# Kernel tuning notes

Hardware: AMD Instinct MI355X
Metric: run time of the kernel (lower is better)

The kernel has to match this reference:

```python
import jax, jax.numpy as jnp
import numpy as np

N_BATCH, D_FEAT, N_CLASSES = 96, 64, 21
MARGIN = 0.3


def setup_inputs() -> dict:
    key = jax.random.key(0)
    k1, k2, k3 = jax.random.split(key, 3)
    logits = jax.random.normal(k1, (N_BATCH, D_FEAT), dtype=jnp.float32)
    feat2 = jax.random.normal(k2, (N_BATCH, D_FEAT), dtype=jnp.float32)
    labels = (jax.random.uniform(k3, (N_BATCH, N_CLASSES)) < 0.3).astype(jnp.float32)
    return {"logits": logits, "labels": labels, "feat2": feat2}


def reference(logits, labels, feat2):
    """Dense-mask formulation of QuadrupletMarginMiner (defaults:
    margin=0.3, type_of_quadruplets='all', what_is_hard='one').

    Instead of a data-dependent list of quadruplets, returns a boolean
    tensor valid[i, j, k, n] that is True exactly for the quadruplets the
    torch module would return (same set, dense encoding).
    """
    n = labels.shape[0]
    eps = 1e-12

    # --- label structure ------------------------------------------------
    s = (labels @ labels.T) > 0                      # share-a-label matrix
    diffs = ~s                                       # torch: sames ^ 1 (pre diag fill)
    sames = s & ~jnp.eye(n, dtype=bool)              # fill_diagonal_(0)
    jk_triu = jnp.triu(jnp.ones((n, n), dtype=bool), k=1)  # strict j < k

    # valid (I, J, K) triples: AP1 & AP2 & j<k   -> [n, n, n]
    triple = sames[:, :, None] & sames[:, None, :] & jk_triu[None, :, :]
    # attach every negative N: diffs[i, n]        -> [n, n, n, n]
    quad = triple[:, :, :, None] & diffs[:, None, None, :]

    # --- distances (negative cosine similarity) ---------------------------
    xn = logits / jnp.maximum(jnp.linalg.norm(logits, axis=1, keepdims=True), eps)
    yn = feat2 / jnp.maximum(jnp.linalg.norm(feat2, axis=1, keepdims=True), eps)
    mat = -(xn @ yn.T)                               # [n, n]

    # margin_p[i, p, neg] = mat[i, neg] - mat[i, p]  (p stands for J or K)
    margin_pn = mat[:, None, :] - mat[:, :, None]    # [i, p, neg]
    viol = margin_pn <= MARGIN                       # [i, p, neg] bool

    # 'all' quadruplets + 'one' hardness: (margin1 <= m) | (margin2 <= m)
    cond = viol[:, :, None, :] | viol[:, None, :, :]  # [i, j, k, neg]

    return quad & cond
```

## Files before the change

### kernel.cpp

```cpp
#include <hip/hip_runtime.h>
#include <math.h>

#define NB 96
#define NB2 (NB * NB)
#define DFEAT 64
#define NCLS 21
#define MARGIN 0.3

typedef int i4 __attribute__((ext_vector_type(4)));
typedef unsigned int u32;

__global__ void precompute_kernel(const float* __restrict__ logits,
                                  const float* __restrict__ labels,
                                  const float* __restrict__ feat2,
                                  double* __restrict__ mat,
                                  double* __restrict__ thr,
                                  unsigned char* __restrict__ share) {
    int gid = blockIdx.x * blockDim.x + threadIdx.x;
    if (gid >= NB2) return;
    int i = gid / NB;
    int j = gid - i * NB;

    const float* xi = logits + i * DFEAT;
    const float* yj = feat2 + j * DFEAT;
    double nx = 0.0, ny = 0.0, dot = 0.0;
#pragma unroll
    for (int d = 0; d < DFEAT; ++d) {
        double a = (double)xi[d];
        double b = (double)yj[d];
        nx += a * a;
        ny += b * b;
        dot += a * b;
    }
    nx = fmax(sqrt(nx), 1e-12);
    ny = fmax(sqrt(ny), 1e-12);
    double m = -(dot / (nx * ny));
    mat[gid] = m;
    thr[gid] = MARGIN + m;

    const float* li = labels + i * NCLS;
    const float* lj = labels + j * NCLS;
    float ldot = 0.f;
#pragma unroll
    for (int c = 0; c < NCLS; ++c) ldot += li[c] * lj[c];
    share[gid] = (ldot > 0.f) ? 1 : 0;
}

__global__ void mask_kernel(const double* __restrict__ mat,
                            const double* __restrict__ thr,
                            const unsigned char* __restrict__ share,
                            u32* __restrict__ mask4) {
    int gid = blockIdx.x * blockDim.x + threadIdx.x;
    if (gid >= NB2) return;
    int i = gid / NB;
    double t = thr[gid];
    const double* mrow = mat + i * NB;
    const unsigned char* srow = share + i * NB;
    u32 w0 = 0, w1 = 0, w2 = 0;
#pragma unroll
    for (int n = 0; n < 32; ++n)
        if (!srow[n] && (mrow[n] <= t)) w0 |= (1u << n);
#pragma unroll
    for (int n = 0; n < 32; ++n)
        if (!srow[32 + n] && (mrow[32 + n] <= t)) w1 |= (1u << n);
#pragma unroll
    for (int n = 0; n < 32; ++n)
        if (!srow[64 + n] && (mrow[64 + n] <= t)) w2 |= (1u << n);
    mask4[gid * 4 + 0] = w0;
    mask4[gid * 4 + 1] = w1;
    mask4[gid * 4 + 2] = w2;
    mask4[gid * 4 + 3] = 0;
}

__global__ __launch_bounds__(256) void quad_kernel(const double* __restrict__ thr,
                                                   const unsigned char* __restrict__ share,
                                                   const u32* __restrict__ mask4,
                                                   int* __restrict__ out) {
    const int bid = blockIdx.x;
    const int i = bid / NB;
    const int j = bid - i * NB;
    const int tid = threadIdx.x;

    __shared__ u32 vrow[NB][4];

    if (tid < NB) {
        const int k = tid;
        const double thr_j = thr[i * NB + j];
        const bool sames_ij = share[i * NB + j] && (j != i);
        const bool ok = sames_ij && share[i * NB + k] && (k != i) && (j < k);
        u32 r0 = 0, r1 = 0, r2 = 0;
        if (ok) {
            int p = (thr[i * NB + k] > thr_j) ? k : j;
            const u32* mp = mask4 + (size_t)(i * NB + p) * 4;
            r0 = mp[0]; r1 = mp[1]; r2 = mp[2];
        }
        vrow[k][0] = r0; vrow[k][1] = r1; vrow[k][2] = r2; vrow[k][3] = 0;
    }
    __syncthreads();

    i4* outp = (i4*)(out + (size_t)bid * (size_t)NB2);

#pragma unroll
    for (int r = 0; r < 9; ++r) {
        int c = r * 256 + tid;
        int k = c / 24;
        int q = c - k * 24;
        u32 w = vrow[k][q >> 3];
        u32 b = w >> ((q & 7) * 4);
        i4 v;
        v.x = (int)(b & 1u);
        v.y = (int)((b >> 1) & 1u);
        v.z = (int)((b >> 2) & 1u);
        v.w = (int)((b >> 3) & 1u);
        __builtin_nontemporal_store(v, &outp[c]);
    }
}

extern "C" void kernel_launch(void* const* d_in, const int* in_sizes, int n_in,
                              void* d_out, int out_size, void* d_ws, size_t ws_size,
                              hipStream_t stream) {
    const float* logits = (const float*)d_in[0];
    const float* labels = (const float*)d_in[1];
    const float* feat2  = (const float*)d_in[2];
    int* out = (int*)d_out;

    double* mat = (double*)d_ws;
    double* thr = mat + NB2;
    unsigned char* share = (unsigned char*)(thr + NB2);
    size_t off = (size_t)(share + NB2 - (unsigned char*)d_ws);
    off = (off + 15) & ~(size_t)15;
    u32* mask4 = (u32*)((unsigned char*)d_ws + off);

    precompute_kernel<<<(NB2 + 255) / 256, 256, 0, stream>>>(logits, labels, feat2,
                                                             mat, thr, share);
    mask_kernel<<<(NB2 + 255) / 256, 256, 0, stream>>>(mat, thr, share, mask4);
    quad_kernel<<<NB2, 256, 0, stream>>>(thr, share, mask4, out);
}
```

Before: 357.9 us.

## Drop thr buffer, stage mask rows in LDS, use regular stores for output

Removes the separate threshold array and computes MARGIN+mat on the fly. The mask kernel now runs one block per row, staging the mat row and the not-share bitmask in shared memory instead of each thread rereading global memory. The quad kernel's output writes switch from nontemporal to regular vector stores. The output write of about 340MB dominates, so the store-type change is the main lever and could help or hurt depending on cache behavior.

```diff
diff --git a/kernel.cpp b/kernel.cpp
--- a/kernel.cpp
+++ b/kernel.cpp
@@ -14,7 +14,6 @@
                                   const float* __restrict__ labels,
                                   const float* __restrict__ feat2,
                                   double* __restrict__ mat,
-                                  double* __restrict__ thr,
                                   unsigned char* __restrict__ share) {
     int gid = blockIdx.x * blockDim.x + threadIdx.x;
     if (gid >= NB2) return;
@@ -34,9 +33,7 @@
     }
     nx = fmax(sqrt(nx), 1e-12);
     ny = fmax(sqrt(ny), 1e-12);
-    double m = -(dot / (nx * ny));
-    mat[gid] = m;
-    thr[gid] = MARGIN + m;
+    mat[gid] = -(dot / (nx * ny));
 
     const float* li = labels + i * NCLS;
     const float* lj = labels + j * NCLS;
@@ -46,33 +43,43 @@
     share[gid] = (ldot > 0.f) ? 1 : 0;
 }
 
-__global__ void mask_kernel(const double* __restrict__ mat,
-                            const double* __restrict__ thr,
-                            const unsigned char* __restrict__ share,
-                            u32* __restrict__ mask4) {
-    int gid = blockIdx.x * blockDim.x + threadIdx.x;
-    if (gid >= NB2) return;
-    int i = gid / NB;
-    double t = thr[gid];
-    const double* mrow = mat + i * NB;
-    const unsigned char* srow = share + i * NB;
+__global__ __launch_bounds__(128) void mask_kernel(const double* __restrict__ mat,
+                                                   const unsigned char* __restrict__ share,
+                                                   u32* __restrict__ mask4) {
+    const int i = blockIdx.x;
+    const int p = threadIdx.x;
+    __shared__ double sm[NB];
+    __shared__ u32 sdiff[3];
+
+    if (p < NB) sm[p] = mat[i * NB + p];
+    if (p < 3) {
+        u32 w = 0;
+        const unsigned char* srow = share + i * NB + p * 32;
+#pragma unroll
+        for (int n = 0; n < 32; ++n)
+            if (!srow[n]) w |= (1u << n);
+        sdiff[p] = w;
+    }
+    __syncthreads();
+    if (p >= NB) return;
+
+    const double t = MARGIN + sm[p];
     u32 w0 = 0, w1 = 0, w2 = 0;
 #pragma unroll
-    for (int n = 0; n < 32; ++n)
-        if (!srow[n] && (mrow[n] <= t)) w0 |= (1u << n);
+    for (int n = 0; n < 32; ++n) if (sm[n] <= t)      w0 |= (1u << n);
 #pragma unroll
-    for (int n = 0; n < 32; ++n)
-        if (!srow[32 + n] && (mrow[32 + n] <= t)) w1 |= (1u << n);
+    for (int n = 0; n < 32; ++n) if (sm[32 + n] <= t) w1 |= (1u << n);
 #pragma unroll
-    for (int n = 0; n < 32; ++n)
-        if (!srow[64 + n] && (mrow[64 + n] <= t)) w2 |= (1u << n);
-    mask4[gid * 4 + 0] = w0;
-    mask4[gid * 4 + 1] = w1;
-    mask4[gid * 4 + 2] = w2;
+    for (int n = 0; n < 32; ++n) if (sm[64 + n] <= t) w2 |= (1u << n);
+
+    const int gid = i * NB + p;
+    mask4[gid * 4 + 0] = w0 & sdiff[0];
+    mask4[gid * 4 + 1] = w1 & sdiff[1];
+    mask4[gid * 4 + 2] = w2 & sdiff[2];
     mask4[gid * 4 + 3] = 0;
 }
 
-__global__ __launch_bounds__(256) void quad_kernel(const double* __restrict__ thr,
+__global__ __launch_bounds__(256) void quad_kernel(const double* __restrict__ mat,
                                                    const unsigned char* __restrict__ share,
                                                    const u32* __restrict__ mask4,
                                                    int* __restrict__ out) {
@@ -85,12 +92,12 @@
 
     if (tid < NB) {
         const int k = tid;
-        const double thr_j = thr[i * NB + j];
+        const double mat_j = mat[i * NB + j];
         const bool sames_ij = share[i * NB + j] && (j != i);
         const bool ok = sames_ij && share[i * NB + k] && (k != i) && (j < k);
         u32 r0 = 0, r1 = 0, r2 = 0;
         if (ok) {
-            int p = (thr[i * NB + k] > thr_j) ? k : j;
+            int p = (mat[i * NB + k] > mat_j) ? k : j;
             const u32* mp = mask4 + (size_t)(i * NB + p) * 4;
             r0 = mp[0]; r1 = mp[1]; r2 = mp[2];
         }
@@ -112,7 +119,7 @@
         v.y = (int)((b >> 1) & 1u);
         v.z = (int)((b >> 2) & 1u);
         v.w = (int)((b >> 3) & 1u);
-        __builtin_nontemporal_store(v, &outp[c]);
+        outp[c] = v;
     }
 }
 
@@ -125,14 +132,13 @@
     int* out = (int*)d_out;
 
     double* mat = (double*)d_ws;
-    double* thr = mat + NB2;
-    unsigned char* share = (unsigned char*)(thr + NB2);
+    unsigned char* share = (unsigned char*)(mat + NB2);
     size_t off = (size_t)(share + NB2 - (unsigned char*)d_ws);
     off = (off + 15) & ~(size_t)15;
     u32* mask4 = (u32*)((unsigned char*)d_ws + off);
 
     precompute_kernel<<<(NB2 + 255) / 256, 256, 0, stream>>>(logits, labels, feat2,
-                                                             mat, thr, share);
-    mask_kernel<<<(NB2 + 255) / 256, 256, 0, stream>>>(mat, thr, share, mask4);
-    quad_kernel<<<NB2, 256, 0, stream>>>(thr, share, mask4, out);
+                                                             mat, share);
+    mask_kernel<<<NB, 128, 0, stream>>>(mat, share, mask4);
+    quad_kernel<<<NB2, 256, 0, stream>>>(mat, share, mask4, out);
 }
```

Measured after the change: 350.3 us. 2.1% less time.
